# Kernel tuning notes

Hardware: AMD Instinct MI355X
Metric: run time of the kernel (lower is better)

The kernel has to match this reference:

```python
import jax, jax.numpy as jnp
import numpy as np

D_MODEL = 1024
D_K = 64
MAX_LEN = 10000
SCALE = float(np.sqrt(2 * D_K))  # TUPE scale sqrt(2*d_k)


def setup_inputs() -> dict:
    key = jax.random.key(0)
    kq, kk, kv, kpe, kuq, kuk = jax.random.split(key, 6)
    b, s = 4, 2048
    q = jax.random.normal(kq, (b, s, D_MODEL), dtype=jnp.float32)
    k = jax.random.normal(kk, (b, s, D_MODEL), dtype=jnp.float32)
    v = jax.random.normal(kv, (b, s, D_MODEL), dtype=jnp.float32)
    # learned PE, uniform(-0.1, 0.1) as in the source
    pe = jax.random.uniform(kpe, (MAX_LEN, D_MODEL), minval=-0.1, maxval=0.1, dtype=jnp.float32)
    # U_q / U_k: Linear(d_model, d_model, bias=False); store as [in, out] so x @ W matches torch x @ W.T convention after transpose choice
    lim = 1.0 / np.sqrt(D_MODEL)
    Uq = jax.random.uniform(kuq, (D_MODEL, D_MODEL), minval=-lim, maxval=lim, dtype=jnp.float32)
    Uk = jax.random.uniform(kuk, (D_MODEL, D_MODEL), minval=-lim, maxval=lim, dtype=jnp.float32)
    return {"q": q, "k": k, "v": v, "pe": pe, "Uq": Uq, "Uk": Uk}


def reference(q, k, v, pe, Uq, Uk):
    b, len_q, d_model = q.shape
    len_k = k.shape[1]
    # NOTE: source computes scores with FULL q/k (over d_model), not per-head.
    scores = jnp.einsum('bqd,bkd->bqk', q, k)  # [b, lq, lk]
    # TUPE positional attention bias
    q_pe = pe[:len_q] @ Uq  # [lq, d]
    k_pe = pe[:len_k] @ Uk  # [lk, d]
    scores = scores + (q_pe @ k_pe.T)[None, :, :]
    scores = scores / SCALE
    attn = jax.nn.softmax(scores, axis=-1)  # dropout p=0 in eval
    context = jnp.einsum('bqk,bkd->bqd', attn, v)  # [b, lq, d_model]
    # replicate torch transpose(1,2).contiguous().view(b, -1, d_model)
    context = jnp.swapaxes(context, 1, 2).reshape(b, -1, d_model)
    return context, attn
```

## Files before the change

### kernel.cpp

```cpp
#include <hip/hip_runtime.h>
#include <hip/hip_bf16.h>
#include <math.h>

#define BATCH 4
#define SEQ   2048
#define DMODEL 1024

typedef __attribute__((ext_vector_type(8))) short bf16x8;
typedef __attribute__((ext_vector_type(4))) float floatx4;

__device__ __forceinline__ void async_copy16(const void* g, void* lds) {
    __builtin_amdgcn_global_load_lds(
        reinterpret_cast<const unsigned int __attribute__((address_space(1)))*>(
            reinterpret_cast<unsigned long long>(g)),
        reinterpret_cast<unsigned int __attribute__((address_space(3)))*>(
            (unsigned int)reinterpret_cast<unsigned long long>(lds)),
        16, 0, 0);
}

#define SCHED_FENCE() __builtin_amdgcn_sched_barrier(0)


#define TILE256(T, U) do {                                                      \
    constexpr int sl  = (U) & 3, sl1 = ((U) + 1) & 3, sl3 = ((U) + 3) & 3;      \
    constexpr int p = (U) & 1, p1 = ((U) + 1) & 1;                              \
                               \
    _Pragma("unroll") for (int i = 0; i < 4; ++i) aH[i] = readA(sl, 4 + i);     \
    stageA((T) + 3, 0, sl3); stageA((T) + 3, 1, sl3);                           \
    asm volatile("s_waitcnt vmcnt(6)" ::: "memory");                            \
    __builtin_amdgcn_s_barrier(); SCHED_FENCE();                                \
    __builtin_amdgcn_s_setprio(1);                                              \
    _Pragma("unroll") for (int i = 0; i < 4; ++i)                               \
      _Pragma("unroll") for (int j = 0; j < 4; ++j)                             \
        acc[i][j] = __builtin_amdgcn_mfma_f32_16x16x32_bf16(aP[p][i], bP[p][j], acc[i][j], 0, 0, 0); \
    __builtin_amdgcn_s_setprio(0);                                              \
                                         \
    _Pragma("unroll") for (int i = 0; i < 4; ++i) aP[p1][i] = readA(sl1, i);    \
    _Pragma("unroll") for (int j = 0; j < 4; ++j) bP[p1][j] = readB(sl1, j);    \
    stageB((T) + 3, 0, sl3); stageB((T) + 3, 1, sl3);                           \
    asm volatile("s_waitcnt lgkmcnt(8)" ::: "memory");                          \
    __builtin_amdgcn_s_barrier(); SCHED_FENCE();                                \
    __builtin_amdgcn_s_setprio(1);                                              \
    _Pragma("unroll") for (int i = 0; i < 4; ++i)                               \
      _Pragma("unroll") for (int j = 0; j < 4; ++j)                             \
        acc[4 + i][j] = __builtin_amdgcn_mfma_f32_16x16x32_bf16(aH[i], bP[p][j], acc[4 + i][j], 0, 0, 0); \
    __builtin_amdgcn_s_setprio(0);                                              \
} while (0)

#define DRAIN256(U, LAST) do {                                                  \
    constexpr int sl = (U) & 3, sl1 = ((U) + 1) & 3;                            \
    constexpr int p = (U) & 1, p1 = ((U) + 1) & 1;                              \
    _Pragma("unroll") for (int i = 0; i < 4; ++i) aH[i] = readA(sl, 4 + i);     \
    _Pragma("unroll") for (int i = 0; i < 4; ++i)                               \
      _Pragma("unroll") for (int j = 0; j < 4; ++j)                             \
        acc[i][j] = __builtin_amdgcn_mfma_f32_16x16x32_bf16(aP[p][i], bP[p][j], acc[i][j], 0, 0, 0); \
    if constexpr (!(LAST)) {                                                    \
        _Pragma("unroll") for (int i = 0; i < 4; ++i) aP[p1][i] = readA(sl1, i);\
        _Pragma("unroll") for (int j = 0; j < 4; ++j) bP[p1][j] = readB(sl1, j);\
    }                                                                           \
    _Pragma("unroll") for (int i = 0; i < 4; ++i)                               \
      _Pragma("unroll") for (int j = 0; j < 4; ++j)                             \
        acc[4 + i][j] = __builtin_amdgcn_mfma_f32_16x16x32_bf16(aH[i], bP[p][j], acc[4 + i][j], 0, 0, 0); \
} while (0)

#define TILE128(T, U) do {                                                      \
    constexpr int sl1 = ((U) + 1) & 3, sl3 = ((U) + 3) & 3;                     \
    constexpr int p = (U) & 1, p1 = ((U) + 1) & 1;                              \
    asm volatile("s_waitcnt vmcnt(3)" ::: "memory");                            \
    __builtin_amdgcn_s_barrier(); SCHED_FENCE();                                \
    _Pragma("unroll") for (int i = 0; i < 8; ++i) aP[p1][i] = readA(sl1, i);    \
    _Pragma("unroll") for (int j = 0; j < 2; ++j) bP[p1][j] = readB(sl1, j);    \
    stageA((T) + 3, 0, sl3); stageA((T) + 3, 1, sl3); stageB((T) + 3, 0, sl3);  \
    asm volatile("s_waitcnt lgkmcnt(10)" ::: "memory");                         \
    __builtin_amdgcn_s_barrier(); SCHED_FENCE();                                \
    __builtin_amdgcn_s_setprio(1);                                              \
    _Pragma("unroll") for (int i = 0; i < 8; ++i)                               \
      _Pragma("unroll") for (int j = 0; j < 2; ++j)                             \
        acc[i][j] = __builtin_amdgcn_mfma_f32_16x16x32_bf16(aP[p][i], bP[p][j], acc[i][j], 0, 0, 0); \
    __builtin_amdgcn_s_setprio(0);                                              \
} while (0)

#define DRAIN128(U, LAST) do {                                                  \
    constexpr int sl1 = ((U) + 1) & 3;                                          \
    constexpr int p = (U) & 1, p1 = ((U) + 1) & 1;                              \
    if constexpr (!(LAST)) {                                                    \
        _Pragma("unroll") for (int i = 0; i < 8; ++i) aP[p1][i] = readA(sl1, i);\
        _Pragma("unroll") for (int j = 0; j < 2; ++j) bP[p1][j] = readB(sl1, j);\
    }                                                                           \
    _Pragma("unroll") for (int i = 0; i < 8; ++i)                               \
      _Pragma("unroll") for (int j = 0; j < 2; ++j)                             \
        acc[i][j] = __builtin_amdgcn_mfma_f32_16x16x32_bf16(aP[p][i], bP[p][j], acc[i][j], 0, 0, 0); \
} while (0)

template<bool ASPLIT, int BN, bool HAS_BIAS, int MM, int NN, int KK, int KBB>
__global__ __launch_bounds__(512, 1)
void gemm8p(const __hip_bfloat16* __restrict__ A0, const __hip_bfloat16* __restrict__ A1,
            const __hip_bfloat16* __restrict__ B, const float* __restrict__ bias,
            float* __restrict__ C, float scale, long sAb, long sBb, long sCb)
{
    constexpr int BM = 256, BK = 32;
    constexpr int NT = KK / BK;
    constexpr int KA = ASPLIT ? (KK / 2) : KK;
    constexpr int WN = BN / 4, NF = WN / 16;
    constexpr int SLOT_A = BM * BK, SLOT_B = BN * BK;
    constexpr int GX = NN / BN, GY = MM / BM;
    constexpr int CPX = (GX * GY) / 8;
    static_assert(NT % 4 == 0 && NT >= 8, "");
    static_assert((GX * GY) % 8 == 0, "");

    __shared__ __align__(16) __hip_bfloat16 sA[4][SLOT_A];
    __shared__ __align__(16) __hip_bfloat16 sB[4][SLOT_B];

    const int bz = blockIdx.z;
    A0 += (long)bz * sAb;
    if (ASPLIT) A1 += (long)bz * sAb;
    B += (long)bz * sBb;
    C += (long)bz * sCb;

    int b = blockIdx.y * GX + blockIdx.x;
    b = (b & 7) * CPX + (b >> 3);
    const int col0 = (b % GX) * BN;
    const int row0 = (b / GX) * BM;

    const int tid  = threadIdx.x;
    const int wave = tid >> 6, lane = tid & 63;
    const int wm = wave >> 2, wn = wave & 3;
    const int fr = lane & 15, fq = lane >> 4;
    const int swz = (fq ^ ((fr >> 1) & 3)) << 3;

    const int s_r  = (wave << 4) + (lane >> 2);
    const int s_c4 = lane & 3;

    auto stageA = [&](int t, int c, int sl) {
        const int lr = (c << 7) + s_r;
        const int ch = (s_c4 ^ ((lr >> 1) & 3)) << 3;
        int k0 = t << 5;
        const __hip_bfloat16* src = A0;
        if (ASPLIT && k0 >= KA) { src = A1; k0 -= KA; }
        async_copy16(src + (long)(row0 + lr) * KA + k0 + ch,
                     &sA[sl][((c << 7) + (wave << 4)) * BK]);
    };
    auto stageB = [&](int t, int c, int sl) {
        const int lr = (c << 7) + s_r;
        const int ch = (s_c4 ^ ((lr >> 1) & 3)) << 3;
        const int k0 = (t << 5) & (KBB - 1);
        async_copy16(B + (long)(col0 + lr) * KBB + k0 + ch,
                     &sB[sl][((c << 7) + (wave << 4)) * BK]);
    };
    auto readA = [&](int sl, int i) -> bf16x8 {
        return *(const bf16x8*)&sA[sl][((wm << 7) + (i << 4) + fr) * BK + swz];
    };
    auto readB = [&](int sl, int j) -> bf16x8 {
        return *(const bf16x8*)&sB[sl][(wn * WN + (j << 4) + fr) * BK + swz];
    };

    floatx4 acc[8][NF];
    #pragma unroll
    for (int i = 0; i < 8; ++i)
        #pragma unroll
        for (int j = 0; j < NF; ++j) acc[i][j] = (floatx4){0.f, 0.f, 0.f, 0.f};

    bf16x8 aP[2][BN == 256 ? 4 : 8];
    bf16x8 bP[2][NF];
    bf16x8 aH[BN == 256 ? 4 : 1];

    if constexpr (BN == 256) {
        stageA(0, 0, 0); stageA(0, 1, 0); stageB(0, 0, 0); stageB(0, 1, 0);
        stageA(1, 0, 1); stageA(1, 1, 1); stageB(1, 0, 1); stageB(1, 1, 1);
        stageA(2, 0, 2); stageA(2, 1, 2); stageB(2, 0, 2); stageB(2, 1, 2);
        asm volatile("s_waitcnt vmcnt(8)" ::: "memory");
        __builtin_amdgcn_s_barrier(); SCHED_FENCE();
        #pragma unroll
        for (int i = 0; i < 4; ++i) aP[0][i] = readA(0, i);
        #pragma unroll
        for (int j = 0; j < 4; ++j) bP[0][j] = readB(0, j);

        #pragma unroll 1
        for (int tt = 0; tt < NT - 4; tt += 4) {
            TILE256(tt + 0, 0); TILE256(tt + 1, 1); TILE256(tt + 2, 2); TILE256(tt + 3, 3);
        }
        TILE256(NT - 4, 0);
        asm volatile("s_waitcnt vmcnt(0)" ::: "memory");
        __builtin_amdgcn_s_barrier(); SCHED_FENCE();
        DRAIN256(1, false); DRAIN256(2, false); DRAIN256(3, true);
    } else {
        stageA(0, 0, 0); stageA(0, 1, 0); stageB(0, 0, 0);
        stageA(1, 0, 1); stageA(1, 1, 1); stageB(1, 0, 1);
        stageA(2, 0, 2); stageA(2, 1, 2); stageB(2, 0, 2);
        asm volatile("s_waitcnt vmcnt(6)" ::: "memory");
        __builtin_amdgcn_s_barrier(); SCHED_FENCE();
        #pragma unroll
        for (int i = 0; i < 8; ++i) aP[0][i] = readA(0, i);
        #pragma unroll
        for (int j = 0; j < 2; ++j) bP[0][j] = readB(0, j);

        #pragma unroll 1
        for (int tt = 0; tt < NT - 4; tt += 4) {
            TILE128(tt + 0, 0); TILE128(tt + 1, 1); TILE128(tt + 2, 2); TILE128(tt + 3, 3);
        }
        TILE128(NT - 4, 0);
        asm volatile("s_waitcnt vmcnt(0)" ::: "memory");
        __builtin_amdgcn_s_barrier(); SCHED_FENCE();
        DRAIN128(1, false); DRAIN128(2, false); DRAIN128(3, true);
    }

    #pragma unroll
    for (int i = 0; i < 8; ++i) {
        #pragma unroll
        for (int r = 0; r < 4; ++r) {
            const int row = row0 + (wm << 7) + (i << 4) + (fq << 2) + r;
            #pragma unroll
            for (int j = 0; j < NF; ++j) {
                const int col = col0 + wn * WN + (j << 4) + fr;
                float val = acc[i][j][r];
                if (HAS_BIAS) val += bias[(long)row * NN + col];
                val *= scale;
                C[(long)row * NN + col] = val;
            }
        }
    }
}

template<bool SPLIT_A, bool HAS_BIAS, bool OUT_TRANS, bool OUT_BF16>
__global__ __launch_bounds__(256, 1)
void mfma_gemm(const __hip_bfloat16* __restrict__ Ah, const __hip_bfloat16* __restrict__ Al,
               const __hip_bfloat16* __restrict__ Bh,
               const float* __restrict__ bias, void* __restrict__ Cvoid,
               int M, int N, int K, float scale,
               long sAb, long sBb, long sCb)
{
    constexpr int NA = SPLIT_A ? 2 : 1;
    __shared__ __align__(16) __hip_bfloat16 sA[NA][128 * 32];
    __shared__ __align__(16) __hip_bfloat16 sB[128 * 32];

    const int bz = blockIdx.z;
    Ah += (long)bz * sAb;
    Bh += (long)bz * sBb;
    if (SPLIT_A) Al += (long)bz * sAb;

    const int row0 = blockIdx.y * 128;
    const int col0 = blockIdx.x * 128;
    const int tid  = threadIdx.x;
    const int wave = tid >> 6;
    const int lane = tid & 63;

    const int srow   = wave * 16 + (lane >> 2);
    const int schunk = (lane & 3) * 8;

    const int wm = (wave >> 1) * 64;
    const int wn = (wave & 1) * 64;
    const int fr = lane & 15;
    const int fk = (lane >> 4) * 8;

    const floatx4 zero = {0.f, 0.f, 0.f, 0.f};
    floatx4 acc[4][4];
    #pragma unroll
    for (int i = 0; i < 4; ++i)
        #pragma unroll
        for (int j = 0; j < 4; ++j) acc[i][j] = zero;

    for (int k0 = 0; k0 < K; k0 += 32) {
        #pragma unroll
        for (int t = 0; t < 2; ++t) {
            const long arow = (long)(row0 + t * 64 + srow);
            const long brow = (long)(col0 + t * 64 + srow);
            const int  soff = (t * 64 + wave * 16) * 32;
            async_copy16(Ah + arow * K + k0 + schunk, &sA[0][soff]);
            async_copy16(Bh + brow * K + k0 + schunk, &sB[soff]);
            if (SPLIT_A)
                async_copy16(Al + arow * K + k0 + schunk, &sA[NA - 1][soff]);
        }
        __syncthreads();

        bf16x8 aH[4], bH[4];
        #pragma unroll
        for (int i = 0; i < 4; ++i) aH[i] = *(const bf16x8*)&sA[0][(wm + i * 16 + fr) * 32 + fk];
        #pragma unroll
        for (int j = 0; j < 4; ++j) bH[j] = *(const bf16x8*)&sB[(wn + j * 16 + fr) * 32 + fk];

        if (SPLIT_A) {
            bf16x8 aL[4];
            #pragma unroll
            for (int i = 0; i < 4; ++i) aL[i] = *(const bf16x8*)&sA[NA - 1][(wm + i * 16 + fr) * 32 + fk];
            #pragma unroll
            for (int i = 0; i < 4; ++i)
                #pragma unroll
                for (int j = 0; j < 4; ++j) {
                    acc[i][j] = __builtin_amdgcn_mfma_f32_16x16x32_bf16(aH[i], bH[j], acc[i][j], 0, 0, 0);
                    acc[i][j] = __builtin_amdgcn_mfma_f32_16x16x32_bf16(aL[i], bH[j], acc[i][j], 0, 0, 0);
                }
        } else {
            #pragma unroll
            for (int i = 0; i < 4; ++i)
                #pragma unroll
                for (int j = 0; j < 4; ++j)
                    acc[i][j] = __builtin_amdgcn_mfma_f32_16x16x32_bf16(aH[i], bH[j], acc[i][j], 0, 0, 0);
        }
        __syncthreads();
    }

    float* Cf = (float*)Cvoid + (long)bz * sCb;
    __hip_bfloat16* Cb = (__hip_bfloat16*)Cvoid + (long)bz * sCb;
    #pragma unroll
    for (int i = 0; i < 4; ++i) {
        #pragma unroll
        for (int r = 0; r < 4; ++r) {
            const int row = row0 + wm + i * 16 + (lane >> 4) * 4 + r;
            #pragma unroll
            for (int j = 0; j < 4; ++j) {
                const int col = col0 + wn + j * 16 + (lane & 15);
                float val = acc[i][j][r];
                if (HAS_BIAS) val += bias[(long)row * N + col];
                val *= scale;
                if (OUT_BF16)       Cb[(long)row * N + col] = __float2bfloat16(val);
                else if (OUT_TRANS) Cf[(long)col * M + row] = val;
                else                Cf[(long)row * N + col] = val;
            }
        }
    }
}

__global__ __launch_bounds__(256)
void convert_bf16_kernel(const float* __restrict__ in, __hip_bfloat16* __restrict__ out, long n)
{
    const long i = ((long)blockIdx.x * 256 + threadIdx.x) * 4;
    if (i >= n) return;
    float va[4];
    *(float4*)va = *(const float4*)(in + i);
    __align__(8) __hip_bfloat16 h[4];
    #pragma unroll
    for (int j = 0; j < 4; ++j) h[j] = __float2bfloat16(va[j]);
    *(uint2*)(out + i) = *(uint2*)h;
}

__global__ __launch_bounds__(256)
void split_convert_kernel(const float* __restrict__ in, __hip_bfloat16* __restrict__ hi,
                          __hip_bfloat16* __restrict__ lo, long n)
{
    const long i = ((long)blockIdx.x * 256 + threadIdx.x) * 4;
    if (i >= n) return;
    float va[4];
    *(float4*)va = *(const float4*)(in + i);
    __align__(8) __hip_bfloat16 h[4], l[4];
    #pragma unroll
    for (int j = 0; j < 4; ++j) {
        h[j] = __float2bfloat16(va[j]);
        l[j] = __float2bfloat16(va[j] - __bfloat162float(h[j]));
    }
    *(uint2*)(hi + i) = *(uint2*)h;
    *(uint2*)(lo + i) = *(uint2*)l;
}

__global__ __launch_bounds__(256)
void transpose_convert_kernel(const float* __restrict__ in, __hip_bfloat16* __restrict__ out,
                              int R, int C, long sIn, long sOut)
{
    in  += (long)blockIdx.z * sIn;
    out += (long)blockIdx.z * sOut;
    __shared__ float t[32][33];
    const int c0 = blockIdx.x * 32, r0 = blockIdx.y * 32;
    for (int i = threadIdx.y; i < 32; i += 8)
        t[i][threadIdx.x] = in[(long)(r0 + i) * C + c0 + threadIdx.x];
    __syncthreads();
    for (int i = threadIdx.y; i < 32; i += 8)
        out[(long)(c0 + i) * R + r0 + threadIdx.x] = __float2bfloat16(t[threadIdx.x][i]);
}

__global__ __launch_bounds__(256)
void softmax_kernel(float* __restrict__ data, __hip_bfloat16* __restrict__ data_bf)
{
    const long row = blockIdx.x;
    float* p = data + row * (long)SEQ;
    __hip_bfloat16* pb = data_bf + row * (long)SEQ;
    const int tid = threadIdx.x;
    const int PER = SEQ / 256;

    float v[PER];
    float m = -1e30f;
    #pragma unroll
    for (int i = 0; i < PER; ++i) {
        v[i] = p[tid + i * 256];
        m = fmaxf(m, v[i]);
    }
    __shared__ float red[256];
    red[tid] = m;
    __syncthreads();
    #pragma unroll
    for (int s = 128; s > 0; s >>= 1) {
        if (tid < s) red[tid] = fmaxf(red[tid], red[tid + s]);
        __syncthreads();
    }
    m = red[0];
    __syncthreads();
    float sum = 0.f;
    #pragma unroll
    for (int i = 0; i < PER; ++i) {
        v[i] = __expf(v[i] - m);
        sum += v[i];
    }
    red[tid] = sum;
    __syncthreads();
    #pragma unroll
    for (int s = 128; s > 0; s >>= 1) {
        if (tid < s) red[tid] += red[tid + s];
        __syncthreads();
    }
    const float inv = 1.0f / red[0];
    #pragma unroll
    for (int i = 0; i < PER; ++i) {
        const float a = v[i] * inv;
        p[tid + i * 256]  = a;
        pb[tid + i * 256] = __float2bfloat16(a);
    }
}

extern "C" void kernel_launch(void* const* d_in, const int* in_sizes, int n_in,
                              void* d_out, int out_size, void* d_ws, size_t ws_size,
                              hipStream_t stream)
{
    const float* q  = (const float*)d_in[0];
    const float* k  = (const float*)d_in[1];
    const float* v  = (const float*)d_in[2];
    const float* pe = (const float*)d_in[3];
    const float* Uq = (const float*)d_in[4];
    const float* Uk = (const float*)d_in[5];

    float* out      = (float*)d_out;
    float* ctx_out  = out;
    float* attn_out = out + (long)BATCH * SEQ * DMODEL;

    const long SD = (long)BATCH * SEQ * DMODEL;
    char* w = (char*)d_ws;
    __hip_bfloat16* q_hi  = (__hip_bfloat16*)w;  w += SD * 2;
    __hip_bfloat16* q_lo  = (__hip_bfloat16*)w;  w += SD * 2;
    __hip_bfloat16* k_bf  = (__hip_bfloat16*)w;  w += SD * 2;
    __hip_bfloat16* pe_bf = (__hip_bfloat16*)w;  w += (long)SEQ * DMODEL * 2;
    __hip_bfloat16* UqT   = (__hip_bfloat16*)w;  w += (long)DMODEL * DMODEL * 2;
    __hip_bfloat16* UkT   = (__hip_bfloat16*)w;  w += (long)DMODEL * DMODEL * 2;
    __hip_bfloat16* qpe_bf= (__hip_bfloat16*)w;  w += (long)SEQ * DMODEL * 2;
    __hip_bfloat16* kpe_bf= (__hip_bfloat16*)w;  w += (long)SEQ * DMODEL * 2;
    float*          biasM = (float*)w;           w += (long)SEQ * SEQ * 4;
    __hip_bfloat16* attn_bf = q_hi;
    __hip_bfloat16* vT      = k_bf;

    const float inv_scale = 1.0f / sqrtf(128.0f);

    convert_bf16_kernel<<<dim3((SEQ * DMODEL) / 4 / 256), 256, 0, stream>>>(pe, pe_bf, (long)SEQ * DMODEL);
    transpose_convert_kernel<<<dim3(DMODEL / 32, DMODEL / 32, 1), dim3(32, 8), 0, stream>>>(
        Uq, UqT, DMODEL, DMODEL, 0, 0);
    transpose_convert_kernel<<<dim3(DMODEL / 32, DMODEL / 32, 1), dim3(32, 8), 0, stream>>>(
        Uk, UkT, DMODEL, DMODEL, 0, 0);
    split_convert_kernel<<<dim3(SD / 4 / 256), 256, 0, stream>>>(q, q_hi, q_lo, SD);
    convert_bf16_kernel<<<dim3(SD / 4 / 256), 256, 0, stream>>>(k, k_bf, SD);

    mfma_gemm<false, false, false, true><<<dim3(DMODEL / 128, SEQ / 128, 2), 256, 0, stream>>>(
        pe_bf, nullptr, UqT, nullptr, qpe_bf, SEQ, DMODEL, DMODEL, 1.0f,
        0, (long)DMODEL * DMODEL, (long)SEQ * DMODEL);

    mfma_gemm<false, false, false, false><<<dim3(SEQ / 128, SEQ / 128, 1), 256, 0, stream>>>(
        qpe_bf, nullptr, kpe_bf, nullptr, biasM, SEQ, SEQ, DMODEL, 1.0f, 0, 0, 0);

    gemm8p<true, 256, true, 2048, 2048, 2048, 1024>
        <<<dim3(SEQ / 256, SEQ / 256, BATCH), 512, 0, stream>>>(
        q_hi, q_lo, k_bf, biasM, attn_out, inv_scale,
        (long)SEQ * DMODEL, (long)SEQ * DMODEL, (long)SEQ * SEQ);

    softmax_kernel<<<dim3(BATCH * SEQ), 256, 0, stream>>>(attn_out, attn_bf);

    transpose_convert_kernel<<<dim3(DMODEL / 32, SEQ / 32, BATCH), dim3(32, 8), 0, stream>>>(
        v, vT, SEQ, DMODEL, (long)SEQ * DMODEL, (long)SEQ * DMODEL);

    gemm8p<false, 128, false, 1024, 2048, 2048, 2048>
        <<<dim3(SEQ / 128, DMODEL / 256, BATCH), 512, 0, stream>>>(
        vT, nullptr, attn_bf, nullptr, ctx_out, 1.0f,
        (long)SEQ * DMODEL, (long)SEQ * SEQ, (long)SEQ * DMODEL);
}
```

Before: 406.8 us.

## Use one barrier per K-tile in the 4-slot LDS GEMM pipeline

Restructures the pipelined GEMM main loop so each K-tile uses a single workgroup barrier at its end instead of two. All global-to-LDS staging for tile T+3 is issued up front. The next fragment LDS reads are overlapped with the second MFMA batch, and the tail is unified into parameterized macros. The goal is to cut barrier stalls and let more MFMA work overlap with memory waits. The tighter vmcnt/lgkmcnt choices risk LDS slot races if the counts are wrong.

```diff
diff --git a/kernel.cpp b/kernel.cpp
--- a/kernel.cpp
+++ b/kernel.cpp
@@ -21,75 +21,56 @@
 #define SCHED_FENCE() __builtin_amdgcn_sched_barrier(0)
 
 
-#define TILE256(T, U) do {                                                      \
-    constexpr int sl  = (U) & 3, sl1 = ((U) + 1) & 3, sl3 = ((U) + 3) & 3;      \
+#define T256(T, U, STG, RA, VMM, BARR) do {                                     \
+    constexpr int sl = (U) & 3, sl1 = ((U) + 1) & 3, sl3 = ((U) + 3) & 3;       \
     constexpr int p = (U) & 1, p1 = ((U) + 1) & 1;                              \
-                               \
     _Pragma("unroll") for (int i = 0; i < 4; ++i) aH[i] = readA(sl, 4 + i);     \
-    stageA((T) + 3, 0, sl3); stageA((T) + 3, 1, sl3);                           \
-    asm volatile("s_waitcnt vmcnt(6)" ::: "memory");                            \
-    __builtin_amdgcn_s_barrier(); SCHED_FENCE();                                \
+    if constexpr (STG) { stageA((T) + 3, 0, sl3); stageA((T) + 3, 1, sl3);      \
+                         stageB((T) + 3, 0, sl3); stageB((T) + 3, 1, sl3); }    \
+    asm volatile("s_waitcnt lgkmcnt(4)" ::: "memory"); SCHED_FENCE();           \
     __builtin_amdgcn_s_setprio(1);                                              \
     _Pragma("unroll") for (int i = 0; i < 4; ++i)                               \
       _Pragma("unroll") for (int j = 0; j < 4; ++j)                             \
         acc[i][j] = __builtin_amdgcn_mfma_f32_16x16x32_bf16(aP[p][i], bP[p][j], acc[i][j], 0, 0, 0); \
     __builtin_amdgcn_s_setprio(0);                                              \
-                                         \
-    _Pragma("unroll") for (int i = 0; i < 4; ++i) aP[p1][i] = readA(sl1, i);    \
-    _Pragma("unroll") for (int j = 0; j < 4; ++j) bP[p1][j] = readB(sl1, j);    \
-    stageB((T) + 3, 0, sl3); stageB((T) + 3, 1, sl3);                           \
-    asm volatile("s_waitcnt lgkmcnt(8)" ::: "memory");                          \
-    __builtin_amdgcn_s_barrier(); SCHED_FENCE();                                \
+    if constexpr (RA) {                                                         \
+        _Pragma("unroll") for (int i = 0; i < 4; ++i) aP[p1][i] = readA(sl1, i);\
+        _Pragma("unroll") for (int j = 0; j < 4; ++j) bP[p1][j] = readB(sl1, j);\
+        asm volatile("s_waitcnt lgkmcnt(8)" ::: "memory");                      \
+    } else {                                                                    \
+        asm volatile("s_waitcnt lgkmcnt(0)" ::: "memory");                      \
+    }                                                                           \
+    SCHED_FENCE();                                                              \
     __builtin_amdgcn_s_setprio(1);                                              \
     _Pragma("unroll") for (int i = 0; i < 4; ++i)                               \
       _Pragma("unroll") for (int j = 0; j < 4; ++j)                             \
         acc[4 + i][j] = __builtin_amdgcn_mfma_f32_16x16x32_bf16(aH[i], bP[p][j], acc[4 + i][j], 0, 0, 0); \
     __builtin_amdgcn_s_setprio(0);                                              \
+    if constexpr ((VMM) == 2)      { asm volatile("s_waitcnt vmcnt(4)" ::: "memory"); } \
+    else if constexpr ((VMM) == 1) { asm volatile("s_waitcnt vmcnt(0)" ::: "memory"); } \
+    if constexpr (BARR) __builtin_amdgcn_s_barrier();                           \
 } while (0)
 
-#define DRAIN256(U, LAST) do {                                                  \
-    constexpr int sl = (U) & 3, sl1 = ((U) + 1) & 3;                            \
-    constexpr int p = (U) & 1, p1 = ((U) + 1) & 1;                              \
-    _Pragma("unroll") for (int i = 0; i < 4; ++i) aH[i] = readA(sl, 4 + i);     \
-    _Pragma("unroll") for (int i = 0; i < 4; ++i)                               \
-      _Pragma("unroll") for (int j = 0; j < 4; ++j)                             \
-        acc[i][j] = __builtin_amdgcn_mfma_f32_16x16x32_bf16(aP[p][i], bP[p][j], acc[i][j], 0, 0, 0); \
-    if constexpr (!(LAST)) {                                                    \
-        _Pragma("unroll") for (int i = 0; i < 4; ++i) aP[p1][i] = readA(sl1, i);\
-        _Pragma("unroll") for (int j = 0; j < 4; ++j) bP[p1][j] = readB(sl1, j);\
-    }                                                                           \
-    _Pragma("unroll") for (int i = 0; i < 4; ++i)                               \
-      _Pragma("unroll") for (int j = 0; j < 4; ++j)                             \
-        acc[4 + i][j] = __builtin_amdgcn_mfma_f32_16x16x32_bf16(aH[i], bP[p][j], acc[4 + i][j], 0, 0, 0); \
-} while (0)
-
-#define TILE128(T, U) do {                                                      \
+#define T128(T, U, STG, RA, VMM, BARR) do {                                     \
     constexpr int sl1 = ((U) + 1) & 3, sl3 = ((U) + 3) & 3;                     \
     constexpr int p = (U) & 1, p1 = ((U) + 1) & 1;                              \
-    asm volatile("s_waitcnt vmcnt(3)" ::: "memory");                            \
-    __builtin_amdgcn_s_barrier(); SCHED_FENCE();                                \
-    _Pragma("unroll") for (int i = 0; i < 8; ++i) aP[p1][i] = readA(sl1, i);    \
-    _Pragma("unroll") for (int j = 0; j < 2; ++j) bP[p1][j] = readB(sl1, j);    \
-    stageA((T) + 3, 0, sl3); stageA((T) + 3, 1, sl3); stageB((T) + 3, 0, sl3);  \
-    asm volatile("s_waitcnt lgkmcnt(10)" ::: "memory");                         \
-    __builtin_amdgcn_s_barrier(); SCHED_FENCE();                                \
+    if constexpr (RA) {                                                         \
+        _Pragma("unroll") for (int i = 0; i < 8; ++i) aP[p1][i] = readA(sl1, i);\
+        _Pragma("unroll") for (int j = 0; j < 2; ++j) bP[p1][j] = readB(sl1, j);\
+    }                                                                           \
+    if constexpr (STG) { stageA((T) + 3, 0, sl3); stageA((T) + 3, 1, sl3);      \
+                         stageB((T) + 3, 0, sl3); }                             \
+    if constexpr (RA) { asm volatile("s_waitcnt lgkmcnt(10)" ::: "memory"); }   \
+    else              { asm volatile("s_waitcnt lgkmcnt(0)" ::: "memory"); }    \
+    SCHED_FENCE();                                                              \
     __builtin_amdgcn_s_setprio(1);                                              \
     _Pragma("unroll") for (int i = 0; i < 8; ++i)                               \
       _Pragma("unroll") for (int j = 0; j < 2; ++j)                             \
         acc[i][j] = __builtin_amdgcn_mfma_f32_16x16x32_bf16(aP[p][i], bP[p][j], acc[i][j], 0, 0, 0); \
     __builtin_amdgcn_s_setprio(0);                                              \
-} while (0)
-
-#define DRAIN128(U, LAST) do {                                                  \
-    constexpr int sl1 = ((U) + 1) & 3;                                          \
-    constexpr int p = (U) & 1, p1 = ((U) + 1) & 1;                              \
-    if constexpr (!(LAST)) {                                                    \
-        _Pragma("unroll") for (int i = 0; i < 8; ++i) aP[p1][i] = readA(sl1, i);\
-        _Pragma("unroll") for (int j = 0; j < 2; ++j) bP[p1][j] = readB(sl1, j);\
-    }                                                                           \
-    _Pragma("unroll") for (int i = 0; i < 8; ++i)                               \
-      _Pragma("unroll") for (int j = 0; j < 2; ++j)                             \
-        acc[i][j] = __builtin_amdgcn_mfma_f32_16x16x32_bf16(aP[p][i], bP[p][j], acc[i][j], 0, 0, 0); \
+    if constexpr ((VMM) == 2)      { asm volatile("s_waitcnt vmcnt(3)" ::: "memory"); } \
+    else if constexpr ((VMM) == 1) { asm volatile("s_waitcnt vmcnt(0)" ::: "memory"); } \
+    if constexpr (BARR) __builtin_amdgcn_s_barrier();                           \
 } while (0)
 
 template<bool ASPLIT, int BN, bool HAS_BIAS, int MM, int NN, int KK, int KBB>
@@ -168,7 +149,7 @@
         stageA(0, 0, 0); stageA(0, 1, 0); stageB(0, 0, 0); stageB(0, 1, 0);
         stageA(1, 0, 1); stageA(1, 1, 1); stageB(1, 0, 1); stageB(1, 1, 1);
         stageA(2, 0, 2); stageA(2, 1, 2); stageB(2, 0, 2); stageB(2, 1, 2);
-        asm volatile("s_waitcnt vmcnt(8)" ::: "memory");
+        asm volatile("s_waitcnt vmcnt(4)" ::: "memory");
         __builtin_amdgcn_s_barrier(); SCHED_FENCE();
         #pragma unroll
         for (int i = 0; i < 4; ++i) aP[0][i] = readA(0, i);
@@ -177,17 +158,18 @@
 
         #pragma unroll 1
         for (int tt = 0; tt < NT - 4; tt += 4) {
-            TILE256(tt + 0, 0); TILE256(tt + 1, 1); TILE256(tt + 2, 2); TILE256(tt + 3, 3);
-        }
-        TILE256(NT - 4, 0);
-        asm volatile("s_waitcnt vmcnt(0)" ::: "memory");
-        __builtin_amdgcn_s_barrier(); SCHED_FENCE();
-        DRAIN256(1, false); DRAIN256(2, false); DRAIN256(3, true);
+            T256(tt + 0, 0, 1, 1, 2, 1); T256(tt + 1, 1, 1, 1, 2, 1);
+            T256(tt + 2, 2, 1, 1, 2, 1); T256(tt + 3, 3, 1, 1, 2, 1);
+        }
+        T256(NT - 4, 0, 1, 1, 2, 1);
+        T256(NT - 3, 1, 0, 1, 1, 1);
+        T256(NT - 2, 2, 0, 1, 0, 0);
+        T256(NT - 1, 3, 0, 0, 0, 0);
     } else {
         stageA(0, 0, 0); stageA(0, 1, 0); stageB(0, 0, 0);
         stageA(1, 0, 1); stageA(1, 1, 1); stageB(1, 0, 1);
         stageA(2, 0, 2); stageA(2, 1, 2); stageB(2, 0, 2);
-        asm volatile("s_waitcnt vmcnt(6)" ::: "memory");
+        asm volatile("s_waitcnt vmcnt(3)" ::: "memory");
         __builtin_amdgcn_s_barrier(); SCHED_FENCE();
         #pragma unroll
         for (int i = 0; i < 8; ++i) aP[0][i] = readA(0, i);
@@ -196,12 +178,13 @@
 
         #pragma unroll 1
         for (int tt = 0; tt < NT - 4; tt += 4) {
-            TILE128(tt + 0, 0); TILE128(tt + 1, 1); TILE128(tt + 2, 2); TILE128(tt + 3, 3);
-        }
-        TILE128(NT - 4, 0);
-        asm volatile("s_waitcnt vmcnt(0)" ::: "memory");
-        __builtin_amdgcn_s_barrier(); SCHED_FENCE();
-        DRAIN128(1, false); DRAIN128(2, false); DRAIN128(3, true);
+            T128(tt + 0, 0, 1, 1, 2, 1); T128(tt + 1, 1, 1, 1, 2, 1);
+            T128(tt + 2, 2, 1, 1, 2, 1); T128(tt + 3, 3, 1, 1, 2, 1);
+        }
+        T128(NT - 4, 0, 1, 1, 2, 1);
+        T128(NT - 3, 1, 0, 1, 1, 1);
+        T128(NT - 2, 2, 0, 1, 0, 0);
+        T128(NT - 1, 3, 0, 0, 0, 0);
     }
 
     #pragma unroll
```

New measurement: 400.0 us. Within noise of the previous version (-1.7%).
